# Optimization experiments

Measured on AMD Instinct MI355X. Metric: run time of the kernel, lower is better.

The kernel has to match this reference:

```python
import jax, jax.numpy as jnp
import numpy as np

B, C_IN, L = 1024, 3, 2048
D, K = 64, 8192          # embedding_dim, num_embeddings
BETA = 0.25
SLOPE = 0.001            # LeakyReLU negative slope


def _leaky(x):
    return jnp.where(x > 0, x, SLOPE * x)


def setup_inputs() -> dict:
    key = jax.random.key(0)
    ks = jax.random.split(key, 16)
    def lin(k, fan_in, shape):  # torch default conv init ~ U(-1/sqrt(fan_in), 1/sqrt(fan_in))
        b = 1.0 / np.sqrt(fan_in)
        return jax.random.uniform(k, shape, jnp.float32, -b, b)
    inp = {
        "x":  jax.random.normal(ks[0], (B, C_IN, L), jnp.float32),
        # encoder conv1x1 weights stored as [out, in]
        "W1": lin(ks[1], C_IN, (64, C_IN)),  "b1": lin(ks[2], C_IN, (64,)),
        "W2": lin(ks[3], 64,   (128, 64)),   "b2": lin(ks[4], 64,  (128,)),
        "W3": lin(ks[5], 128,  (D, 128)),    "b3": lin(ks[6], 128, (D,)),
        # codebook init: uniform(-1/K, 1/K) as in the torch module
        "codebook": jax.random.uniform(ks[7], (K, D), jnp.float32, -1.0 / K, 1.0 / K),
        # decoder convtranspose1x1 weights stored as [in, out]
        "U1": lin(ks[8],  D,   (D, 128)),    "c1": lin(ks[9],  D,   (128,)),
        "U2": lin(ks[10], 128, (128, 64)),   "c2": lin(ks[11], 128, (64,)),
        "U3": lin(ks[12], 64,  (64, C_IN)),  "c3": lin(ks[13], 64,  (C_IN,)),
    }
    return inp


def reference(x, W1, b1, W2, b2, W3, b3, codebook, U1, c1, U2, c2, U3, c3):
    # ---- encoder: conv1x1 stack over [B, C, L] then global max pool ----
    h = _leaky(jnp.einsum('oc,bcl->bol', W1, x) + b1[None, :, None])   # [B,64,L]
    h = _leaky(jnp.einsum('oc,bcl->bol', W2, h) + b2[None, :, None])   # [B,128,L]
    h = jnp.einsum('oc,bcl->bol', W3, h) + b3[None, :, None]           # [B,D,L]
    z = jnp.max(h, axis=-1)                                            # [B,D]

    # ---- vector quantizer ----
    d = (jnp.sum(z * z, axis=1, keepdims=True)
         + jnp.sum(codebook * codebook, axis=1)
         - 2.0 * z @ codebook.T)                                       # [B,K]
    idx = jnp.argmin(d, axis=1)                                        # [B]
    z_q = codebook[idx]                                                # [B,D]
    sg = jax.lax.stop_gradient
    loss = jnp.mean((sg(z_q) - z) ** 2) + BETA * jnp.mean((z_q - sg(z)) ** 2)
    z_q_st = z + sg(z_q - z)                                           # straight-through

    # ---- decoder: convtranspose1x1 on length-1 sequence == dense layers ----
    g = _leaky(z_q_st @ U1 + c1)                                       # [B,128]
    g = _leaky(g @ U2 + c2)                                            # [B,64]
    x_recon = (g @ U3 + c3)[:, :, None]                                # [B,3,1]
    return x_recon, loss, z
```

## Files before the change

kernel.cpp:

```cpp
#include <hip/hip_runtime.h>
#include <hip/hip_bf16.h>

#define BB 1024
#define LL 2048
#define KK 8192

typedef _Float16 f16x8 __attribute__((ext_vector_type(8)));
typedef _Float16 f16x4 __attribute__((ext_vector_type(4)));
typedef _Float16 f16x2 __attribute__((ext_vector_type(2)));
typedef float    f32x4 __attribute__((ext_vector_type(4)));

__device__ __forceinline__ float leakyf(float v){ return fmaxf(v, 0.001f*v); }
__device__ __forceinline__ f16x2 pkrtz(float a, float b){
    return __builtin_bit_cast(f16x2, __builtin_amdgcn_cvt_pkrtz(a, b));
}

__global__ __launch_bounds__(256, 2) void encoder_mfma(
    const float* __restrict__ x,
    const float* __restrict__ W1, const float* __restrict__ b1,
    const float* __restrict__ W2, const float* __restrict__ b2,
    const float* __restrict__ W3, const float* __restrict__ b3,
    float* __restrict__ z_out, _Float16* __restrict__ zh_out)
{
    const int b    = blockIdx.x;
    const int t    = threadIdx.x;
    const int wave = t >> 6;
    const int lane = t & 63;
    const int col  = lane & 15;
    const int quad = lane >> 4;

    __shared__ __align__(16) _Float16 h2lds[4*16*136];
    __shared__ float red[4][64];

    f16x8 w2f[2][8];
    #pragma unroll
    for (int ks=0; ks<2; ks++){
        #pragma unroll
        for (int nt=0; nt<8; nt++){
            const float* p = W2 + (nt*16+col)*64 + quad*8 + 32*ks;
            f16x8 f;
            #pragma unroll
            for (int j=0;j<8;j++) f[j] = (_Float16)p[j];
            w2f[ks][nt] = f;
        }
    }
    f16x8 w3f[4][4];
    #pragma unroll
    for (int ks=0; ks<4; ks++){
        #pragma unroll
        for (int nt=0; nt<4; nt++){
            const float* p = W3 + (nt*16+col)*128 + quad*8 + 32*ks;
            f16x8 f;
            #pragma unroll
            for (int j=0;j<8;j++) f[j] = (_Float16)p[j];
            w3f[ks][nt] = f;
        }
    }
    f16x2 w1p[2][4][3];
    f16x2 b1p[2][4];
    #pragma unroll
    for (int ks=0; ks<2; ks++){
        #pragma unroll
        for (int j2=0; j2<4; j2++){
            int c0 = quad*8 + 2*j2 + 32*ks;
            #pragma unroll
            for (int i=0;i<3;i++){
                f16x2 w; w[0] = (_Float16)W1[c0*3+i]; w[1] = (_Float16)W1[(c0+1)*3+i];
                w1p[ks][j2][i] = w;
            }
            f16x2 bb; bb[0] = (_Float16)b1[c0]; bb[1] = (_Float16)b1[c0+1];
            b1p[ks][j2] = bb;
        }
    }
    f16x2 b2p[8];
    #pragma unroll
    for (int nt=0; nt<8; nt++){
        _Float16 bv = (_Float16)b2[nt*16+col];
        f16x2 p; p[0]=bv; p[1]=bv; b2p[nt]=p;
    }

    f16x2 k001; k001[0] = (_Float16)0.001f; k001[1] = (_Float16)0.001f;
    f32x4 zc; zc[0]=0.f; zc[1]=0.f; zc[2]=0.f; zc[3]=0.f;

    f32x4 hm[4];
    #pragma unroll
    for (int nt=0;nt<4;nt++){
        hm[nt][0] = -__builtin_inff(); hm[nt][1] = -__builtin_inff();
        hm[nt][2] = -__builtin_inff(); hm[nt][3] = -__builtin_inff();
    }

    const float* xb = x + (size_t)b*3*LL;
    const int wave_off = wave*2176;
    const int pbase = wave*16 + col;
    const int rswz  = (col >> 2) << 4;

    float x0n = xb[pbase], x1n = xb[LL+pbase], x2n = xb[2*LL+pbase];

    #pragma unroll 1
    for (int it=0; it<LL/64; it++){
        const float x0 = x0n, x1 = x1n, x2 = x2n;
        {
            int itn = it+1 < 32 ? it+1 : 31;
            int pn = itn*64 + pbase;
            x0n = xb[pn]; x1n = xb[LL+pn]; x2n = xb[2*LL+pn];
        }
        f16x2 xh0; xh0[0] = (_Float16)x0; xh0[1] = xh0[0];
        f16x2 xh1; xh1[0] = (_Float16)x1; xh1[1] = xh1[0];
        f16x2 xh2; xh2[0] = (_Float16)x2; xh2[1] = xh2[0];

        f16x8 a2[2];
        #pragma unroll
        for (int ks=0; ks<2; ks++){
            f16x8 a;
            #pragma unroll
            for (int j2=0; j2<4; j2++){
                f16x2 v = b1p[ks][j2];
                v += w1p[ks][j2][0]*xh0;
                v += w1p[ks][j2][1]*xh1;
                v += w1p[ks][j2][2]*xh2;
                v = __builtin_elementwise_max(v, v*k001);
                a[2*j2]   = v[0];
                a[2*j2+1] = v[1];
            }
            a2[ks] = a;
        }

        #pragma unroll
        for (int ph=0; ph<2; ph++){
            #pragma unroll
            for (int n=0; n<4; n++){
                const int nt = ph*4 + n;
                f32x4 acc = __builtin_amdgcn_mfma_f32_16x16x32_f16(a2[0], w2f[0][nt], zc, 0,0,0);
                acc = __builtin_amdgcn_mfma_f32_16x16x32_f16(a2[1], w2f[1][nt], acc, 0,0,0);
                f16x2 p01 = pkrtz(acc[0], acc[1]);
                f16x2 p23 = pkrtz(acc[2], acc[3]);
                p01 += b2p[nt];  p23 += b2p[nt];
                p01 = __builtin_elementwise_max(p01, p01*k001);
                p23 = __builtin_elementwise_max(p23, p23*k001);
                _Float16* wp = &h2lds[wave_off + quad*4*136 + ((nt ^ quad)<<4) + col];
                wp[0]     = p01[0];
                wp[136]   = p01[1];
                wp[272]   = p23[0];
                wp[408]   = p23[1];
            }
        }

        f16x8 a30 = *(const f16x8*)&h2lds[wave_off + col*136 + (( 0 + quad*8) ^ rswz)];
        f16x8 a31 = *(const f16x8*)&h2lds[wave_off + col*136 + ((32 + quad*8) ^ rswz)];
        f16x8 a32 = *(const f16x8*)&h2lds[wave_off + col*136 + ((64 + quad*8) ^ rswz)];
        f16x8 a33 = *(const f16x8*)&h2lds[wave_off + col*136 + ((96 + quad*8) ^ rswz)];
        #pragma unroll
        for (int nt=0; nt<4; nt++){
            f32x4 acc = __builtin_amdgcn_mfma_f32_16x16x32_f16(a30, w3f[0][nt], zc, 0,0,0);
            acc = __builtin_amdgcn_mfma_f32_16x16x32_f16(a31, w3f[1][nt], acc, 0,0,0);
            acc = __builtin_amdgcn_mfma_f32_16x16x32_f16(a32, w3f[2][nt], acc, 0,0,0);
            acc = __builtin_amdgcn_mfma_f32_16x16x32_f16(a33, w3f[3][nt], acc, 0,0,0);
            hm[nt][0] = fmaxf(hm[nt][0], acc[0]);
            hm[nt][1] = fmaxf(hm[nt][1], acc[1]);
            hm[nt][2] = fmaxf(hm[nt][2], acc[2]);
            hm[nt][3] = fmaxf(hm[nt][3], acc[3]);
        }
    }

    #pragma unroll
    for (int nt=0; nt<4; nt++){
        float v = fmaxf(fmaxf(hm[nt][0], hm[nt][1]), fmaxf(hm[nt][2], hm[nt][3]));
        v = fmaxf(v, __shfl_xor(v, 16, 64));
        v = fmaxf(v, __shfl_xor(v, 32, 64));
        if (quad == 0) red[wave][nt*16 + col] = v;
    }
    __syncthreads();
    if (t < 64){
        float v = fmaxf(fmaxf(red[0][t], red[1][t]), fmaxf(red[2][t], red[3][t])) + b3[t];
        z_out[(size_t)b*64 + t] = v;
        zh_out[(size_t)b*64 + t] = (_Float16)v;
    }
}

__global__ __launch_bounds__(256, 2) void vq_prep(
    const float* __restrict__ cb, _Float16* __restrict__ cbh, float* __restrict__ cnorm)
{
    const int t = threadIdx.x;
    const int wave = t >> 6, lane = t & 63;
    const int e   = blockIdx.x*16 + wave*4 + (lane >> 4);
    const int sub = lane & 15;
    const float4 v = *(const float4*)(cb + (size_t)e*64 + sub*4);
    f16x2 h0 = pkrtz(v.x, v.y);
    f16x2 h1 = pkrtz(v.z, v.w);
    f16x4 hv; hv[0]=h0[0]; hv[1]=h0[1]; hv[2]=h1[0]; hv[3]=h1[1];
    *(f16x4*)(cbh + (size_t)e*64 + sub*4) = hv;
    float d = v.x*v.x + v.y*v.y + v.z*v.z + v.w*v.w;
    #pragma unroll
    for (int s=1; s<16; s<<=1) d += __shfl_xor(d, s, 64);
    if (sub == 0) cnorm[e] = d;
}

__global__ __launch_bounds__(256, 2) void vq_mfma(
    const _Float16* __restrict__ zh, const _Float16* __restrict__ cbh,
    const float* __restrict__ cnorm,
    float* __restrict__ pval, int* __restrict__ pidx)
{
    const int t    = threadIdx.x;
    const int wave = t >> 6;
    const int lane = t & 63;
    const int col  = lane & 15;
    const int quad = lane >> 4;
    const int rb   = blockIdx.x >> 5;
    const int ns   = blockIdx.x & 31;
    const int rowbase = rb*64 + wave*16;

    f16x8 az[2];
    az[0] = *(const f16x8*)&zh[(size_t)(rowbase+col)*64 + quad*8];
    az[1] = *(const f16x8*)&zh[(size_t)(rowbase+col)*64 + quad*8 + 32];

    float best[4] = {__builtin_inff(),__builtin_inff(),__builtin_inff(),__builtin_inff()};
    int   bidx[4] = {0,0,0,0};

    int e = ns*256;
    f16x8 bf0 = *(const f16x8*)&cbh[(size_t)(e+col)*64 + quad*8];
    f16x8 bf1 = *(const f16x8*)&cbh[(size_t)(e+col)*64 + quad*8 + 32];
    float cn  = cnorm[e+col];

    #pragma unroll 1
    for (int nt=0; nt<16; nt++){
        f16x8 c0 = bf0, c1 = bf1;
        float cnc = cn;
        int ec = e;
        if (nt < 15){
            e += 16;
            bf0 = *(const f16x8*)&cbh[(size_t)(e+col)*64 + quad*8];
            bf1 = *(const f16x8*)&cbh[(size_t)(e+col)*64 + quad*8 + 32];
            cn  = cnorm[e+col];
        }
        f32x4 acc; acc[0]=0.f; acc[1]=0.f; acc[2]=0.f; acc[3]=0.f;
        acc = __builtin_amdgcn_mfma_f32_16x16x32_f16(az[0], c0, acc, 0,0,0);
        acc = __builtin_amdgcn_mfma_f32_16x16x32_f16(az[1], c1, acc, 0,0,0);
        int myidx = ec + col;
        #pragma unroll
        for (int r=0; r<4; r++){
            float d = fmaf(-2.0f, acc[r], cnc);
            if (d < best[r]){ best[r] = d; bidx[r] = myidx; }
        }
    }

    #pragma unroll
    for (int r=0; r<4; r++){
        float v = best[r]; int i = bidx[r];
        #pragma unroll
        for (int s=1; s<16; s<<=1){
            float ov = __shfl_xor(v, s, 64);
            int   oi = __shfl_xor(i, s, 64);
            if (ov < v || (ov == v && oi < i)){ v = ov; i = oi; }
        }
        if (col == 0){
            int row = rowbase + quad*4 + r;
            pval[row*32 + ns] = v;
            pidx[row*32 + ns] = i;
        }
    }
}

__global__ __launch_bounds__(128, 2) void decoder_kernel(
    const float* __restrict__ z,
    const float* __restrict__ pval, const int* __restrict__ pidx,
    const float* __restrict__ cb,
    const float* __restrict__ U1, const float* __restrict__ c1,
    const float* __restrict__ U2, const float* __restrict__ c2,
    const float* __restrict__ U3, const float* __restrict__ c3,
    float* __restrict__ xrec, float* __restrict__ loss_part)
{
    const int b = blockIdx.x;
    const int t = threadIdx.x;
    __shared__ int kk_s;
    __shared__ float zst[64];
    __shared__ float g1[128];
    __shared__ float g2[64];
    if (t < 32){
        float v = pval[b*32 + t]; int i = pidx[b*32 + t];
        #pragma unroll
        for (int s=1; s<32; s<<=1){
            float ov = __shfl_xor(v, s, 32);
            int   oi = __shfl_xor(i, s, 32);
            if (ov < v || (ov == v && oi < i)){ v = ov; i = oi; }
        }
        if (t==0) kk_s = i;
    }
    __syncthreads();
    const int kk = kk_s;
    if (t < 64){
        float zv = z[(size_t)b*64 + t];
        float zq = cb[(size_t)kk*64 + t];
        float diff = zq - zv;
        zst[t] = zv + diff;
        float p = diff*diff;
        #pragma unroll
        for (int s=32;s>0;s>>=1) p += __shfl_xor(p, s, 64);
        if (t==0) loss_part[b] = p;
    }
    __syncthreads();
    {
        float v = c1[t];
        #pragma unroll
        for (int d=0; d<64; d++) v = fmaf(zst[d], U1[d*128+t], v);
        g1[t] = leakyf(v);
    }
    __syncthreads();
    if (t < 64){
        float v = c2[t];
        #pragma unroll
        for (int j=0;j<128;j++) v = fmaf(g1[j], U2[j*64+t], v);
        g2[t] = leakyf(v);
    }
    __syncthreads();
    if (t < 3){
        float v = c3[t];
        #pragma unroll
        for (int j=0;j<64;j++) v = fmaf(g2[j], U3[j*3+t], v);
        xrec[(size_t)b*3 + t] = v;
    }
}

__global__ __launch_bounds__(256, 1) void loss_kernel(
    const float* __restrict__ loss_part, float* __restrict__ out)
{
    const int t = threadIdx.x;
    float s = 0.f;
    for (int i=t;i<BB;i+=256) s += loss_part[i];
    #pragma unroll
    for (int sh=32;sh>0;sh>>=1) s += __shfl_xor(s, sh, 64);
    __shared__ float w[4];
    if ((t&63)==0) w[t>>6] = s;
    __syncthreads();
    if (t==0) out[0] = (w[0]+w[1]+w[2]+w[3]) * (1.25f / 65536.0f);
}

extern "C" void kernel_launch(void* const* d_in, const int* in_sizes, int n_in,
                              void* d_out, int out_size, void* d_ws, size_t ws_size,
                              hipStream_t stream)
{
    const float* x  = (const float*)d_in[0];
    const float* W1 = (const float*)d_in[1];
    const float* b1 = (const float*)d_in[2];
    const float* W2 = (const float*)d_in[3];
    const float* b2 = (const float*)d_in[4];
    const float* W3 = (const float*)d_in[5];
    const float* b3 = (const float*)d_in[6];
    const float* cb = (const float*)d_in[7];
    const float* U1 = (const float*)d_in[8];
    const float* c1 = (const float*)d_in[9];
    const float* U2 = (const float*)d_in[10];
    const float* c2 = (const float*)d_in[11];
    const float* U3 = (const float*)d_in[12];
    const float* c3 = (const float*)d_in[13];

    float* out  = (float*)d_out;
    float* xrec = out;
    float* loss = out + 3072;
    float* z    = out + 3073;

    char* ws = (char*)d_ws;
    float*    lp    = (float*)ws;
    _Float16* zh    = (_Float16*)(ws + 4096);
    float*    cnorm = (float*)(ws + 135168);
    float*    pval  = (float*)(ws + 167936);
    int*      pidx  = (int*)(ws + 299008);
    _Float16* cbh   = (_Float16*)(ws + 430080);

    hipLaunchKernelGGL(vq_prep, dim3(512), dim3(256), 0, stream, cb, cbh, cnorm);
    hipLaunchKernelGGL(encoder_mfma, dim3(BB), dim3(256), 0, stream,
                       x, W1, b1, W2, b2, W3, b3, z, zh);
    hipLaunchKernelGGL(vq_mfma, dim3(512), dim3(256), 0, stream, zh, cbh, cnorm, pval, pidx);
    hipLaunchKernelGGL(decoder_kernel, dim3(BB), dim3(128), 0, stream,
                       z, pval, pidx, cb, U1, c1, U2, c2, U3, c3, xrec, lp);
    hipLaunchKernelGGL(loss_kernel, dim3(1), dim3(256), 0, stream, lp, loss);
}
```

Baseline: 226.2 us.

## Fuse codebook prep into VQ kernel via LDS staging; pin encoder weights in AGPRs

Removes the separate vq_prep launch. Each VQ block now converts its 256-entry codebook slice to fp16 and computes the norms into LDS, then runs the MFMA distance loop from LDS. This saves a kernel launch and a global round trip, at the cost of redundant conversion: each slice is recomputed by 16 row-blocks. The encoder also switches to inline-asm MFMA that takes weight fragments from AGPRs, to ease VGPR pressure, and flattens the layer-2 loop.

New measurement: 211.4 us. 1.07x faster.

```diff
diff --git a/kernel.cpp b/kernel.cpp
--- a/kernel.cpp
+++ b/kernel.cpp
@@ -13,6 +13,12 @@
 __device__ __forceinline__ float leakyf(float v){ return fmaxf(v, 0.001f*v); }
 __device__ __forceinline__ f16x2 pkrtz(float a, float b){
     return __builtin_bit_cast(f16x2, __builtin_amdgcn_cvt_pkrtz(a, b));
+}
+__device__ __forceinline__ f32x4 mfma_w(f16x8 a, f16x8 w_agpr, f32x4 c){
+    f32x4 d;
+    asm("v_mfma_f32_16x16x32_f16 %0, %1, %2, %3"
+        : "=v"(d) : "v"(a), "a"(w_agpr), "v"(c));
+    return d;
 }
 
 __global__ __launch_bounds__(256, 2) void encoder_mfma(
@@ -126,23 +132,19 @@
         }
 
         #pragma unroll
-        for (int ph=0; ph<2; ph++){
-            #pragma unroll
-            for (int n=0; n<4; n++){
-                const int nt = ph*4 + n;
-                f32x4 acc = __builtin_amdgcn_mfma_f32_16x16x32_f16(a2[0], w2f[0][nt], zc, 0,0,0);
-                acc = __builtin_amdgcn_mfma_f32_16x16x32_f16(a2[1], w2f[1][nt], acc, 0,0,0);
-                f16x2 p01 = pkrtz(acc[0], acc[1]);
-                f16x2 p23 = pkrtz(acc[2], acc[3]);
-                p01 += b2p[nt];  p23 += b2p[nt];
-                p01 = __builtin_elementwise_max(p01, p01*k001);
-                p23 = __builtin_elementwise_max(p23, p23*k001);
-                _Float16* wp = &h2lds[wave_off + quad*4*136 + ((nt ^ quad)<<4) + col];
-                wp[0]     = p01[0];
-                wp[136]   = p01[1];
-                wp[272]   = p23[0];
-                wp[408]   = p23[1];
-            }
+        for (int nt=0; nt<8; nt++){
+            f32x4 acc = mfma_w(a2[0], w2f[0][nt], zc);
+            acc = mfma_w(a2[1], w2f[1][nt], acc);
+            f16x2 p01 = pkrtz(acc[0], acc[1]);
+            f16x2 p23 = pkrtz(acc[2], acc[3]);
+            p01 += b2p[nt];  p23 += b2p[nt];
+            p01 = __builtin_elementwise_max(p01, p01*k001);
+            p23 = __builtin_elementwise_max(p23, p23*k001);
+            _Float16* wp = &h2lds[wave_off + quad*4*136 + ((nt ^ quad)<<4) + col];
+            wp[0]     = p01[0];
+            wp[136]   = p01[1];
+            wp[272]   = p23[0];
+            wp[408]   = p23[1];
         }
 
         f16x8 a30 = *(const f16x8*)&h2lds[wave_off + col*136 + (( 0 + quad*8) ^ rswz)];
@@ -151,10 +153,10 @@
         f16x8 a33 = *(const f16x8*)&h2lds[wave_off + col*136 + ((96 + quad*8) ^ rswz)];
         #pragma unroll
         for (int nt=0; nt<4; nt++){
-            f32x4 acc = __builtin_amdgcn_mfma_f32_16x16x32_f16(a30, w3f[0][nt], zc, 0,0,0);
-            acc = __builtin_amdgcn_mfma_f32_16x16x32_f16(a31, w3f[1][nt], acc, 0,0,0);
-            acc = __builtin_amdgcn_mfma_f32_16x16x32_f16(a32, w3f[2][nt], acc, 0,0,0);
-            acc = __builtin_amdgcn_mfma_f32_16x16x32_f16(a33, w3f[3][nt], acc, 0,0,0);
+            f32x4 acc = mfma_w(a30, w3f[0][nt], zc);
+            acc = mfma_w(a31, w3f[1][nt], acc);
+            acc = mfma_w(a32, w3f[2][nt], acc);
+            acc = mfma_w(a33, w3f[3][nt], acc);
             hm[nt][0] = fmaxf(hm[nt][0], acc[0]);
             hm[nt][1] = fmaxf(hm[nt][1], acc[1]);
             hm[nt][2] = fmaxf(hm[nt][2], acc[2]);
@@ -177,27 +179,8 @@
     }
 }
 
-__global__ __launch_bounds__(256, 2) void vq_prep(
-    const float* __restrict__ cb, _Float16* __restrict__ cbh, float* __restrict__ cnorm)
-{
-    const int t = threadIdx.x;
-    const int wave = t >> 6, lane = t & 63;
-    const int e   = blockIdx.x*16 + wave*4 + (lane >> 4);
-    const int sub = lane & 15;
-    const float4 v = *(const float4*)(cb + (size_t)e*64 + sub*4);
-    f16x2 h0 = pkrtz(v.x, v.y);
-    f16x2 h1 = pkrtz(v.z, v.w);
-    f16x4 hv; hv[0]=h0[0]; hv[1]=h0[1]; hv[2]=h1[0]; hv[3]=h1[1];
-    *(f16x4*)(cbh + (size_t)e*64 + sub*4) = hv;
-    float d = v.x*v.x + v.y*v.y + v.z*v.z + v.w*v.w;
-    #pragma unroll
-    for (int s=1; s<16; s<<=1) d += __shfl_xor(d, s, 64);
-    if (sub == 0) cnorm[e] = d;
-}
-
 __global__ __launch_bounds__(256, 2) void vq_mfma(
-    const _Float16* __restrict__ zh, const _Float16* __restrict__ cbh,
-    const float* __restrict__ cnorm,
+    const _Float16* __restrict__ zh, const float* __restrict__ cb,
     float* __restrict__ pval, int* __restrict__ pidx)
 {
     const int t    = threadIdx.x;
@@ -207,35 +190,45 @@
     const int quad = lane >> 4;
     const int rb   = blockIdx.x >> 5;
     const int ns   = blockIdx.x & 31;
+
+    __shared__ __align__(16) _Float16 cbl[256*72];
+    __shared__ float cnl[256];
+
+    const int eoff = wave*4 + (lane >> 4);
+    const int sub  = lane & 15;
+    #pragma unroll 4
+    for (int p=0; p<16; p++){
+        const int el = p*16 + eoff;
+        const float4 v = *(const float4*)(cb + ((size_t)(ns*256 + el))*64 + sub*4);
+        f16x2 h0 = pkrtz(v.x, v.y);
+        f16x2 h1 = pkrtz(v.z, v.w);
+        f16x4 hv; hv[0]=h0[0]; hv[1]=h0[1]; hv[2]=h1[0]; hv[3]=h1[1];
+        *(f16x4*)(cbl + el*72 + sub*4) = hv;
+        float d = v.x*v.x + v.y*v.y + v.z*v.z + v.w*v.w;
+        #pragma unroll
+        for (int s=1; s<16; s<<=1) d += __shfl_xor(d, s, 64);
+        if (sub == 0) cnl[el] = d;
+    }
+    __syncthreads();
+
     const int rowbase = rb*64 + wave*16;
-
     f16x8 az[2];
     az[0] = *(const f16x8*)&zh[(size_t)(rowbase+col)*64 + quad*8];
     az[1] = *(const f16x8*)&zh[(size_t)(rowbase+col)*64 + quad*8 + 32];
 
+    f32x4 zc; zc[0]=0.f; zc[1]=0.f; zc[2]=0.f; zc[3]=0.f;
     float best[4] = {__builtin_inff(),__builtin_inff(),__builtin_inff(),__builtin_inff()};
     int   bidx[4] = {0,0,0,0};
 
-    int e = ns*256;
-    f16x8 bf0 = *(const f16x8*)&cbh[(size_t)(e+col)*64 + quad*8];
-    f16x8 bf1 = *(const f16x8*)&cbh[(size_t)(e+col)*64 + quad*8 + 32];
-    float cn  = cnorm[e+col];
-
-    #pragma unroll 1
+    #pragma unroll 4
     for (int nt=0; nt<16; nt++){
-        f16x8 c0 = bf0, c1 = bf1;
-        float cnc = cn;
-        int ec = e;
-        if (nt < 15){
-            e += 16;
-            bf0 = *(const f16x8*)&cbh[(size_t)(e+col)*64 + quad*8];
-            bf1 = *(const f16x8*)&cbh[(size_t)(e+col)*64 + quad*8 + 32];
-            cn  = cnorm[e+col];
-        }
-        f32x4 acc; acc[0]=0.f; acc[1]=0.f; acc[2]=0.f; acc[3]=0.f;
-        acc = __builtin_amdgcn_mfma_f32_16x16x32_f16(az[0], c0, acc, 0,0,0);
+        const int el = nt*16 + col;
+        f16x8 c0 = *(const f16x8*)&cbl[el*72 + quad*8];
+        f16x8 c1 = *(const f16x8*)&cbl[el*72 + quad*8 + 32];
+        float cnc = cnl[el];
+        f32x4 acc = __builtin_amdgcn_mfma_f32_16x16x32_f16(az[0], c0, zc, 0,0,0);
         acc = __builtin_amdgcn_mfma_f32_16x16x32_f16(az[1], c1, acc, 0,0,0);
-        int myidx = ec + col;
+        const int myidx = ns*256 + el;
         #pragma unroll
         for (int r=0; r<4; r++){
             float d = fmaf(-2.0f, acc[r], cnc);
@@ -361,15 +354,12 @@
     char* ws = (char*)d_ws;
     float*    lp    = (float*)ws;
     _Float16* zh    = (_Float16*)(ws + 4096);
-    float*    cnorm = (float*)(ws + 135168);
-    float*    pval  = (float*)(ws + 167936);
-    int*      pidx  = (int*)(ws + 299008);
-    _Float16* cbh   = (_Float16*)(ws + 430080);
-
-    hipLaunchKernelGGL(vq_prep, dim3(512), dim3(256), 0, stream, cb, cbh, cnorm);
+    float*    pval  = (float*)(ws + 135168);
+    int*      pidx  = (int*)(ws + 266240);
+
     hipLaunchKernelGGL(encoder_mfma, dim3(BB), dim3(256), 0, stream,
                        x, W1, b1, W2, b2, W3, b3, z, zh);
-    hipLaunchKernelGGL(vq_mfma, dim3(512), dim3(256), 0, stream, zh, cbh, cnorm, pval, pidx);
+    hipLaunchKernelGGL(vq_mfma, dim3(512), dim3(256), 0, stream, zh, cb, pval, pidx);
     hipLaunchKernelGGL(decoder_kernel, dim3(BB), dim3(128), 0, stream,
                        z, pval, pidx, cb, U1, c1, U2, c2, U3, c3, xrec, lp);
     hipLaunchKernelGGL(loss_kernel, dim3(1), dim3(256), 0, stream, lp, loss);
```
